# Optimization experiments

Measured on AMD Instinct MI355X. Metric: run time of the kernel, lower is better.

## Reference

```python
import jax, jax.numpy as jnp
import numpy as np

B, L, E, H = 2, 2048, 1024, 16
HD = E // H          # head_dim = 64
G = H // 4           # heads per kernel-size group = 4


def _dwconv(x, w, b):
    """Causal depthwise conv. x: (B, G, L, D); w: (D, k); b: (D,).
    Matches PadLeft(k-1) + Conv1d(D, D, k, groups=D): y[l] = sum_j w[:, j] * x[l - (k-1) + j] + b."""
    k = w.shape[-1]
    Lx = x.shape[2]
    xp = jnp.pad(x, ((0, 0), (0, 0), (k - 1, 0), (0, 0)))
    out = b
    for j in range(k):
        out = out + xp[:, :, j:j + Lx, :] * w[:, j]
    return out


def setup_inputs() -> dict:
    key = jax.random.key(0)
    ks = jax.random.split(key, 32)
    s = 0.02
    inp = {"x": jax.random.normal(ks[0], (B, L, E), jnp.float32)}
    for i, n in enumerate(["Wq", "Wk", "Wv", "Wo"]):
        inp[n] = jax.random.normal(ks[1 + i], (E, E), jnp.float32) * s
    inp["bo"] = jax.random.normal(ks[5], (E,), jnp.float32) * s
    i = 6
    for ksz in (3, 5, 7):
        for pfx in ("q", "k", "v"):
            inp[f"{pfx}{ksz}_w"] = jax.random.normal(ks[i], (HD, ksz), jnp.float32) * (1.0 / ksz)
            inp[f"{pfx}{ksz}_b"] = jax.random.normal(ks[i + 1], (HD,), jnp.float32) * s
            i += 2
    return inp


def reference(x, Wq, Wk, Wv, Wo, bo,
              q3_w, q3_b, k3_w, k3_b, v3_w, v3_b,
              q5_w, q5_b, k5_w, k5_b, v5_w, v5_b,
              q7_w, q7_b, k7_w, k7_b, v7_w, v7_b):
    b, l, _ = x.shape

    def split(t):  # (b, l, E) -> (b, 4, G, l, HD)
        return t.reshape(b, l, 4, G, HD).transpose(0, 2, 3, 1, 4)

    q = split(x @ Wq.T)
    k = split(x @ Wk.T)
    v = split(x @ Wv.T)

    # NOTE: faithful to source quirks -- k and v convs are applied to the
    # (already convolved) q group, not to k/v.
    q0, k0, v0 = q[:, 0], k[:, 0], v[:, 0]
    q1 = _dwconv(q[:, 1], q3_w, q3_b)
    k1 = _dwconv(q1, k3_w, k3_b)
    v1 = _dwconv(q1, v3_w, v3_b)
    q2 = _dwconv(q[:, 2], q5_w, q5_b)
    k2 = _dwconv(q2, k5_w, k5_b)
    v2 = _dwconv(q2, v5_w, v5_b)
    q3 = _dwconv(q[:, 3], q7_w, q7_b)
    k3 = _dwconv(q3, k7_w, k7_b)
    v3 = _dwconv(q3, v7_w, v7_b)

    Q = jnp.concatenate([q0, q1, q2, q3], axis=1)  # (b, H, l, HD)
    K = jnp.concatenate([k0, k1, k2, k3], axis=1)
    V = jnp.concatenate([v0, v1, v2, v3], axis=1)

    logit = jnp.einsum('bnid,bnjd->bnij', Q, K) * (HD ** -0.5)
    attn = jax.nn.softmax(logit, axis=-1)
    attn_out = jnp.einsum('bnij,bnjd->bnid', attn, V)

    # Source quirk: output uses rearranged V, discarding attn_out.
    out = V.transpose(0, 2, 1, 3).reshape(b, l, E)
    # keep the attention compute alive without changing the math
    out = out + 0.0 * attn_out.transpose(0, 2, 1, 3).reshape(b, l, E)
    return out @ Wo.T + bo
```

## Files before the change

kernel.cpp:

```cpp
#include <hip/hip_runtime.h>
#include <hip/hip_bf16.h>
#include <stdint.h>

#define L_SEQ 2048
#define MTOT  4096
#define EDIM  1024

typedef __attribute__((ext_vector_type(8))) short bf16x8;
typedef __attribute__((ext_vector_type(4))) float f32x4;
typedef __attribute__((ext_vector_type(16))) float f32x16;
typedef __attribute__((ext_vector_type(4))) float float4v;
typedef __attribute__((ext_vector_type(4))) unsigned short us4;

__device__ __forceinline__ unsigned short f2b(float f) {
    union { float f; unsigned u; } v; v.f = f;
    return (unsigned short)((v.u + 0x7FFFu + ((v.u >> 16) & 1u)) >> 16);
}
__device__ __forceinline__ float b2f(unsigned short h) {
    union { unsigned u; float f; } v; v.u = ((unsigned)h) << 16;
    return v.f;
}
__device__ __forceinline__ unsigned cvtpk(float lo, float hi) {
    unsigned r;
    asm("v_cvt_pk_bf16_f32 %0, %1, %2" : "=v"(r) : "v"(lo), "v"(hi));
    return r;
}
__device__ __forceinline__ void lds16(const void* g, void* l) {
    __builtin_amdgcn_global_load_lds((const __attribute__((address_space(1))) void*)g,
                                     (__attribute__((address_space(3))) void*)l, 16, 0, 0);
}

__global__ __launch_bounds__(256) void wprep_kernel(
    const float* __restrict__ Wq, const float* __restrict__ Wv,
    const float* __restrict__ Wo,
    unsigned short* __restrict__ W1b, unsigned short* __restrict__ Wob,
    const float* __restrict__ q3w, const float* __restrict__ q3b,
    const float* __restrict__ v3w, const float* __restrict__ v3b,
    const float* __restrict__ q5w, const float* __restrict__ q5b,
    const float* __restrict__ v5w, const float* __restrict__ v5b,
    const float* __restrict__ q7w, const float* __restrict__ q7b,
    const float* __restrict__ v7w, const float* __restrict__ v7b,
    float* __restrict__ H, float* __restrict__ Beff, float* __restrict__ Corr)
{
    if (blockIdx.x >= 2048) {
        int ch = (blockIdx.x - 2048) * 256 + threadIdx.x;
        int g = ch >> 8, d = ch & 63, k = 3 + 2 * g;
        const float* qw = (g == 0) ? q3w : (g == 1) ? q5w : q7w;
        const float* qb = (g == 0) ? q3b : (g == 1) ? q5b : q7b;
        const float* vw = (g == 0) ? v3w : (g == 1) ? v5w : v7w;
        const float* vb = (g == 0) ? v3b : (g == 1) ? v5b : v7b;

        float hq[7], hv[7];
        for (int i = 0; i < 7; ++i) { hq[i] = 0.f; hv[i] = 0.f; }
        for (int i = 0; i < k; ++i) {
            hq[i] = qw[d * k + (k - 1 - i)];
            hv[i] = vw[d * k + (k - 1 - i)];
        }
        float h[13];
        for (int i = 0; i < 13; ++i) h[i] = 0.f;
        for (int a = 0; a < 7; ++a)
            for (int b = 0; b < 7; ++b)
                h[a + b] += hq[a] * hv[b];
        for (int i = 0; i < 13; ++i) H[i * 768 + ch] = h[i];

        float sv = 0.f;
        for (int j = 0; j < k; ++j) sv += vw[d * k + j];
        Beff[ch] = qb[d] * sv + vb[d];

        for (int l = 0; l < 6; ++l) {
            float s2 = 0.f;
            for (int i = l + 1; i < 7; ++i) s2 += hv[i];
            Corr[l * 768 + ch] = qb[d] * s2;
        }
        return;
    }
    const int WQ = (EDIM * EDIM) / 4;
    int i = blockIdx.x * 256 + threadIdx.x;
    const float* src;
    unsigned short* dst;
    int j;
    if (i < WQ) {
        j = i * 4;
        int row = j >> 10;
        src = (row < 256) ? Wv : Wq;
        dst = W1b;
    } else {
        j = (i - WQ) * 4; src = Wo; dst = Wob;
    }
    float4v v = *(const float4v*)(src + j);
    us4 o;
    o[0] = f2b(v[0]); o[1] = f2b(v[1]); o[2] = f2b(v[2]); o[3] = f2b(v[3]);
    *(us4*)(dst + j) = o;
}

__global__ __launch_bounds__(512, 2) void gemm1_fused(
    const float* __restrict__ Af, const unsigned short* __restrict__ BT,
    unsigned short* __restrict__ V,
    const float* __restrict__ H, const float* __restrict__ Beff,
    const float* __restrict__ Corr)
{
    constexpr int ABUF = 49152, ABYT = 32768;
    __shared__ uint8_t sh[3 * ABUF];

    int orig = blockIdx.y * 8 + blockIdx.x;
    int wg   = (orig & 7) * 32 + (orig >> 3);
    const int m0 = (wg >> 3) * 128, n0 = (wg & 7) * 128;
    const bool fir = (n0 >= 256);
    const int  m0h = (m0 == 0) ? 0 : (m0 - 32);
    const int  lbase = m0 & (L_SEQ - 1);

    const int tid  = threadIdx.x;
    const int wid  = tid >> 6;
    const int lane = tid & 63;
    const int wr   = wid >> 2;
    const int wc   = (wid >> 1) & 1;
    const int kh   = wid & 1;
    const int l31  = lane & 31, hi = lane >> 5;
    const bool firw = fir && (wr == 0);

    f32x16 acc[2][2] = {};
    f32x16 hacc[2] = {};

    f32x4 h0s0a = {}, h0s0b = {}, h0s1a = {}, h0s1b = {};
    f32x4 h1s0a = {}, h1s0b = {}, h1s1a = {}, h1s1b = {};
    const float* hrow = Af + (size_t)(m0h + l31) * EDIM + kh * 32 + hi * 8;

#define HALOLOAD(B, t) do { if (firw) {                                     \
        const float* hp = hrow + (t) * 64;                                  \
        h##B##s0a = *(const f32x4*)(hp);      h##B##s0b = *(const f32x4*)(hp + 4);  \
        h##B##s1a = *(const f32x4*)(hp + 16); h##B##s1b = *(const f32x4*)(hp + 20); } } while (0)

    auto stage = [&](int buf, int t) {
        uint8_t* Abase = sh + buf * ABUF;
        uint8_t* Bbase = Abase + ABYT;
        const float* Asrc = Af + (size_t)m0 * EDIM + t * 64;
#pragma unroll
        for (int j = 0; j < 4; ++j) {
            int slot = j * 512 + tid;
            int row = slot >> 4, c = (slot & 15) ^ (row & 15);
            lds16(Asrc + (size_t)row * EDIM + c * 4, Abase + j * 8192 + wid * 1024);
        }
        const unsigned short* Bsrc = BT + (size_t)n0 * EDIM + t * 64;
#pragma unroll
        for (int j = 0; j < 2; ++j) {
            int slot = j * 512 + tid;
            int row = slot >> 3, c = (slot & 7) ^ (row & 7);
            lds16(Bsrc + (size_t)row * EDIM + c * 8, Bbase + j * 8192 + wid * 1024);
        }
    };

    auto compute = [&](int buf, f32x4 hs0a, f32x4 hs0b, f32x4 hs1a, f32x4 hs1b) {
        const uint8_t* Abase = sh + buf * ABUF;
        const unsigned short* bs = (const unsigned short*)(Abase + ABYT);
#pragma unroll
        for (int s = 0; s < 2; ++s) {
            bf16x8 a[2], b[2];
#pragma unroll
            for (int mi = 0; mi < 2; ++mi) {
                int row = wr * 64 + mi * 32 + l31;
                const float* as = (const float*)Abase;
                int c0 = kh * 8 + s * 4 + hi * 2;
                f32x4 lo = *(const f32x4*)(as + row * 64 + ((c0 ^ (row & 15)) * 4));
                f32x4 h4 = *(const f32x4*)(as + row * 64 + (((c0 + 1) ^ (row & 15)) * 4));
                union { unsigned u[4]; bf16x8 v; } fu;
                fu.u[0] = cvtpk(lo[0], lo[1]); fu.u[1] = cvtpk(lo[2], lo[3]);
                fu.u[2] = cvtpk(h4[0], h4[1]); fu.u[3] = cvtpk(h4[2], h4[3]);
                a[mi] = fu.v;
            }
#pragma unroll
            for (int ni = 0; ni < 2; ++ni) {
                int row = wc * 64 + ni * 32 + l31;
                int cg = kh * 4 + s * 2 + hi;
                b[ni] = *(const bf16x8*)(bs + row * 64 + ((cg ^ (row & 7)) * 8));
            }
#pragma unroll
            for (int mi = 0; mi < 2; ++mi)
#pragma unroll
                for (int ni = 0; ni < 2; ++ni)
                    acc[mi][ni] = __builtin_amdgcn_mfma_f32_32x32x16_bf16(a[mi], b[ni], acc[mi][ni], 0, 0, 0);
            if (firw) {
                f32x4 pa = s ? hs1a : hs0a, pb = s ? hs1b : hs0b;
                union { unsigned u[4]; bf16x8 v; } hu;
                hu.u[0] = cvtpk(pa[0], pa[1]); hu.u[1] = cvtpk(pa[2], pa[3]);
                hu.u[2] = cvtpk(pb[0], pb[1]); hu.u[3] = cvtpk(pb[2], pb[3]);
                hacc[0] = __builtin_amdgcn_mfma_f32_32x32x16_bf16(hu.v, b[0], hacc[0], 0, 0, 0);
                hacc[1] = __builtin_amdgcn_mfma_f32_32x32x16_bf16(hu.v, b[1], hacc[1], 0, 0, 0);
            }
        }
    };

    const int NT = EDIM >> 6;
    HALOLOAD(0, 0);
    stage(0, 0);
    stage(1, 1);
    asm volatile("s_waitcnt vmcnt(6)" ::: "memory");
    __builtin_amdgcn_s_barrier();
    asm volatile("" ::: "memory");

    for (int tt = 0; tt < NT; tt += 2) {
        HALOLOAD(1, tt + 1);
        if (tt + 2 < NT) stage((tt + 2) % 3, tt + 2);
        compute(tt % 3, h0s0a, h0s0b, h0s1a, h0s1b);
        if (tt + 2 < NT) asm volatile("s_waitcnt vmcnt(6)" ::: "memory");
        else             asm volatile("s_waitcnt vmcnt(0)" ::: "memory");
        __builtin_amdgcn_s_barrier();
        asm volatile("" ::: "memory");
        if (tt + 2 < NT) HALOLOAD(0, tt + 2);
        if (tt + 3 < NT) stage((tt + 3) % 3, tt + 3);
        compute((tt + 1) % 3, h1s0a, h1s0b, h1s1a, h1s1b);
        if (tt + 2 < NT) {
            if (tt + 3 < NT) asm volatile("s_waitcnt vmcnt(6)" ::: "memory");
            else             asm volatile("s_waitcnt vmcnt(0)" ::: "memory");
            __builtin_amdgcn_s_barrier();
            asm volatile("" ::: "memory");
        }
    }
#undef HALOLOAD

    __syncthreads();
    float* Mg = (float*)sh;
    const int mgbase = (wr * 2 + wc) * 4096;
    if (kh) {
#pragma unroll
        for (int mi = 0; mi < 2; ++mi)
#pragma unroll
            for (int ni = 0; ni < 2; ++ni) {
                int col = ni * 32 + l31;
#pragma unroll
                for (int q = 0; q < 4; ++q) {
                    int grp = mi * 8 + 2 * q + hi;
                    int adr = mgbase + col * 64 + (((grp) ^ (col & 15)) << 2);
                    f32x4 v;
                    v[0] = acc[mi][ni][q * 4 + 0]; v[1] = acc[mi][ni][q * 4 + 1];
                    v[2] = acc[mi][ni][q * 4 + 2]; v[3] = acc[mi][ni][q * 4 + 3];
                    *(f32x4*)(Mg + adr) = v;
                }
            }
        if (firw) {
#pragma unroll
            for (int ni = 0; ni < 2; ++ni) {
                int hcol = ni * 32 + l31;
#pragma unroll
                for (int q = 0; q < 4; ++q) {
                    int hg = 2 * q + hi;
                    int adr = 16384 + wc * 2048 + hcol * 32 + ((hg ^ (hcol & 7)) << 2);
                    f32x4 v;
                    v[0] = hacc[ni][q * 4 + 0]; v[1] = hacc[ni][q * 4 + 1];
                    v[2] = hacc[ni][q * 4 + 2]; v[3] = hacc[ni][q * 4 + 3];
                    *(f32x4*)(Mg + adr) = v;
                }
            }
        }
    }
    __syncthreads();
    if (fir) {
        unsigned short* Tl = (unsigned short*)(sh + 81920);
        if (!kh) {
#pragma unroll
            for (int mi = 0; mi < 2; ++mi)
#pragma unroll
                for (int ni = 0; ni < 2; ++ni) {
                    int col = wc * 64 + ni * 32 + l31;
#pragma unroll
                    for (int q = 0; q < 4; ++q) {
                        int grp = mi * 8 + 2 * q + hi;
                        int adr = mgbase + (ni * 32 + l31) * 64 + (((grp) ^ ((ni * 32 + l31) & 15)) << 2);
                        f32x4 p = *(const f32x4*)(Mg + adr);
                        int Lr = 32 + wr * 64 + mi * 32 + 8 * q + 4 * hi;
                        us4 o;
#pragma unroll
                        for (int j = 0; j < 4; ++j) o[j] = f2b(acc[mi][ni][q * 4 + j] + p[j]);
                        *(us4*)(Tl + col * 172 + Lr) = o;
                    }
                }
            if (wr == 0) {
#pragma unroll
                for (int ni = 0; ni < 2; ++ni) {
                    int hcol = ni * 32 + l31;
                    int col = wc * 64 + hcol;
#pragma unroll
                    for (int q = 0; q < 4; ++q) {
                        int hg = 2 * q + hi;
                        int adr = 16384 + wc * 2048 + hcol * 32 + ((hg ^ (hcol & 7)) << 2);
                        f32x4 p = *(const f32x4*)(Mg + adr);
                        int Lr = 8 * q + 4 * hi;
                        us4 o;
#pragma unroll
                        for (int j = 0; j < 4; ++j) o[j] = f2b(hacc[ni][q * 4 + j] + p[j]);
                        *(us4*)(Tl + col * 172 + Lr) = o;
                    }
                }
            }
        }
        __syncthreads();
        int c = tid & 127, rb = tid >> 7;
        int ch = n0 + c - 256;
        float h[13];
#pragma unroll
        for (int i = 0; i < 13; ++i) h[i] = H[i * 768 + ch];
        float beff = Beff[ch];
        const unsigned short* wp = Tl + c * 172 + 20 + rb * 32;
        float wf[44];
#pragma unroll
        for (int j = 0; j < 11; ++j) {
            us4 t4 = *(const us4*)(wp + j * 4);
            wf[j * 4 + 0] = b2f(t4[0]); wf[j * 4 + 1] = b2f(t4[1]);
            wf[j * 4 + 2] = b2f(t4[2]); wf[j * 4 + 3] = b2f(t4[3]);
        }
        if (lbase == 0 && rb == 0) {
#pragma unroll
            for (int j = 0; j < 12; ++j) wf[j] = 0.f;
        }
        unsigned short* vp = V + (size_t)(m0 + rb * 32) * EDIM + n0 + c;
#pragma unroll
        for (int rr = 0; rr < 32; ++rr) {
            float s = beff;
#pragma unroll
            for (int i = 0; i < 13; ++i) s += h[i] * wf[12 + rr - i];
            int l = lbase + rb * 32 + rr;
            if (l < 6) s -= Corr[l * 768 + ch];
            vp[(size_t)rr * EDIM] = f2b(s);
        }
    } else {
        if (!kh) {
#pragma unroll
            for (int mi = 0; mi < 2; ++mi) {
#pragma unroll
                for (int ni = 0; ni < 2; ++ni) {
                    int col = ni * 32 + l31;
                    int gcol = n0 + wc * 64 + col;
#pragma unroll
                    for (int q = 0; q < 4; ++q) {
                        int grp = mi * 8 + 2 * q + hi;
                        int adr = mgbase + col * 64 + (((grp) ^ (col & 15)) << 2);
                        f32x4 p = *(const f32x4*)(Mg + adr);
                        int rowb = m0 + wr * 64 + mi * 32 + 8 * q + 4 * hi;
#pragma unroll
                        for (int j = 0; j < 4; ++j)
                            V[(size_t)(rowb + j) * EDIM + gcol] = f2b(acc[mi][ni][q * 4 + j] + p[j]);
                    }
                }
            }
        }
    }
}

__global__ __launch_bounds__(512, 2) void gemm2_k(
    const unsigned short* __restrict__ Ab, const unsigned short* __restrict__ BT,
    float* __restrict__ Cf, const float* __restrict__ bias)
{
    constexpr int ABUF = 32768, ABYT = 16384;
    __shared__ uint8_t sh[3 * ABUF];

    int orig = blockIdx.y * 8 + blockIdx.x;
    int wg   = (orig & 7) * 32 + (orig >> 3);
    const int m0 = (wg >> 3) * 128, n0 = (wg & 7) * 128;

    const int tid  = threadIdx.x;
    const int wid  = tid >> 6;
    const int lane = tid & 63;
    const int wr   = wid >> 2;
    const int wc   = (wid >> 1) & 1;
    const int kh   = wid & 1;
    const int l31  = lane & 31, hi = lane >> 5;

    f32x16 acc[2][2] = {};

    auto stage = [&](int buf, int t) {
        uint8_t* Abase = sh + buf * ABUF;
        uint8_t* Bbase = Abase + ABYT;
        const unsigned short* Asrc = Ab + (size_t)m0 * EDIM + t * 64;
#pragma unroll
        for (int j = 0; j < 2; ++j) {
            int slot = j * 512 + tid;
            int row = slot >> 3, c = (slot & 7) ^ (row & 7);
            lds16(Asrc + (size_t)row * EDIM + c * 8, Abase + j * 8192 + wid * 1024);
        }
        const unsigned short* Bsrc = BT + (size_t)n0 * EDIM + t * 64;
#pragma unroll
        for (int j = 0; j < 2; ++j) {
            int slot = j * 512 + tid;
            int row = slot >> 3, c = (slot & 7) ^ (row & 7);
            lds16(Bsrc + (size_t)row * EDIM + c * 8, Bbase + j * 8192 + wid * 1024);
        }
    };

    auto compute = [&](int buf) {
        const uint8_t* Abase = sh + buf * ABUF;
        const unsigned short* as = (const unsigned short*)Abase;
        const unsigned short* bs = (const unsigned short*)(Abase + ABYT);
#pragma unroll
        for (int s = 0; s < 2; ++s) {
            bf16x8 a[2], b[2];
#pragma unroll
            for (int mi = 0; mi < 2; ++mi) {
                int row = wr * 64 + mi * 32 + l31;
                int cg = kh * 4 + s * 2 + hi;
                a[mi] = *(const bf16x8*)(as + row * 64 + ((cg ^ (row & 7)) * 8));
            }
#pragma unroll
            for (int ni = 0; ni < 2; ++ni) {
                int row = wc * 64 + ni * 32 + l31;
                int cg = kh * 4 + s * 2 + hi;
                b[ni] = *(const bf16x8*)(bs + row * 64 + ((cg ^ (row & 7)) * 8));
            }
#pragma unroll
            for (int mi = 0; mi < 2; ++mi)
#pragma unroll
                for (int ni = 0; ni < 2; ++ni)
                    acc[mi][ni] = __builtin_amdgcn_mfma_f32_32x32x16_bf16(a[mi], b[ni], acc[mi][ni], 0, 0, 0);
        }
    };

    const int NT = EDIM >> 6;
    stage(0, 0);
    stage(1, 1);
    asm volatile("s_waitcnt vmcnt(4)" ::: "memory");
    __builtin_amdgcn_s_barrier();
    asm volatile("" ::: "memory");

    for (int t = 0; t < NT; ++t) {
        if (t + 2 < NT) stage((t + 2) % 3, t + 2);
        compute(t % 3);
        if (t + 1 < NT) {
            if (t + 2 < NT) asm volatile("s_waitcnt vmcnt(4)" ::: "memory");
            else            asm volatile("s_waitcnt vmcnt(0)" ::: "memory");
            __builtin_amdgcn_s_barrier();
            asm volatile("" ::: "memory");
        }
    }

    __syncthreads();
    float* Mg = (float*)sh;
    const int mgbase = (wr * 2 + wc) * 4096;
    if (kh) {
#pragma unroll
        for (int mi = 0; mi < 2; ++mi)
#pragma unroll
            for (int ni = 0; ni < 2; ++ni) {
                int col = ni * 32 + l31;
#pragma unroll
                for (int q = 0; q < 4; ++q) {
                    int grp = mi * 8 + 2 * q + hi;
                    int adr = mgbase + col * 64 + (((grp) ^ (col & 15)) << 2);
                    f32x4 v;
                    v[0] = acc[mi][ni][q * 4 + 0]; v[1] = acc[mi][ni][q * 4 + 1];
                    v[2] = acc[mi][ni][q * 4 + 2]; v[3] = acc[mi][ni][q * 4 + 3];
                    *(f32x4*)(Mg + adr) = v;
                }
            }
    }
    __syncthreads();
    if (!kh) {
#pragma unroll
        for (int mi = 0; mi < 2; ++mi) {
#pragma unroll
            for (int ni = 0; ni < 2; ++ni) {
                int col = ni * 32 + l31;
                int gcol = n0 + wc * 64 + col;
#pragma unroll
                for (int q = 0; q < 4; ++q) {
                    int grp = mi * 8 + 2 * q + hi;
                    int adr = mgbase + col * 64 + (((grp) ^ (col & 15)) << 2);
                    f32x4 p = *(const f32x4*)(Mg + adr);
                    int rowb = m0 + wr * 64 + mi * 32 + 8 * q + 4 * hi;
#pragma unroll
                    for (int j = 0; j < 4; ++j)
                        Cf[(size_t)(rowb + j) * EDIM + gcol] = acc[mi][ni][q * 4 + j] + p[j] + bias[gcol];
                }
            }
        }
    }
}

extern "C" void kernel_launch(void* const* d_in, const int* in_sizes, int n_in,
                              void* d_out, int out_size, void* d_ws, size_t ws_size,
                              hipStream_t stream)
{
    const float* x  = (const float*)d_in[0];
    const float* Wq = (const float*)d_in[1];
    const float* Wv = (const float*)d_in[3];
    const float* Wo = (const float*)d_in[4];
    const float* bo = (const float*)d_in[5];

    uint8_t* ws = (uint8_t*)d_ws;
    unsigned short* W1b = (unsigned short*)(ws);
    unsigned short* Wob = (unsigned short*)(ws + (2u  << 20));
    unsigned short* V   = (unsigned short*)(ws + (4u  << 20));
    float* H    = (float*)(ws + (12u << 20));
    float* Beff = (float*)(ws + (12u << 20) + (64u << 10));
    float* Corr = (float*)(ws + (12u << 20) + (96u << 10));

    wprep_kernel<<<2051, 256, 0, stream>>>(
        Wq, Wv, Wo, W1b, Wob,
        (const float*)d_in[6],  (const float*)d_in[7],
        (const float*)d_in[10], (const float*)d_in[11],
        (const float*)d_in[12], (const float*)d_in[13],
        (const float*)d_in[16], (const float*)d_in[17],
        (const float*)d_in[18], (const float*)d_in[19],
        (const float*)d_in[22], (const float*)d_in[23],
        H, Beff, Corr);

    dim3 gg(EDIM / 128, MTOT / 128);
    gemm1_fused<<<gg, 512, 0, stream>>>(x, W1b, V, H, Beff, Corr);

    gemm2_k<<<gg, 512, 0, stream>>>(V, Wob, (float*)d_out, bo);
}
```

Before: 53.85 us.

## Fuse weight bf16 conversion and conv-filter prep into the GEMM kernels

Removes the separate wprep kernel that converted Wq/Wv/Wo to bf16 and precomputed the composed conv filters. gemm1 now loads fp32 weights into registers, converts them to bf16 and writes them to LDS in its software pipeline, and computes the filter taps and bias corrections inline in the epilogue. gemm2 stages fp32 Wo directly into LDS via global_load_lds and converts when reading fragments, which increases its LDS footprint and wait counts. This saves one launch and a pass over the weights, but every tile re-converts weights and moves twice the bytes for the B operand.

```diff
diff --git a/kernel.cpp b/kernel.cpp
--- a/kernel.cpp
+++ b/kernel.cpp
@@ -9,7 +9,6 @@
 typedef __attribute__((ext_vector_type(8))) short bf16x8;
 typedef __attribute__((ext_vector_type(4))) float f32x4;
 typedef __attribute__((ext_vector_type(16))) float f32x16;
-typedef __attribute__((ext_vector_type(4))) float float4v;
 typedef __attribute__((ext_vector_type(4))) unsigned short us4;
 
 __device__ __forceinline__ unsigned short f2b(float f) {
@@ -30,74 +29,16 @@
                                      (__attribute__((address_space(3))) void*)l, 16, 0, 0);
 }
 
-__global__ __launch_bounds__(256) void wprep_kernel(
-    const float* __restrict__ Wq, const float* __restrict__ Wv,
-    const float* __restrict__ Wo,
-    unsigned short* __restrict__ W1b, unsigned short* __restrict__ Wob,
+__global__ __launch_bounds__(512, 2) void gemm1_fused(
+    const float* __restrict__ Af, const float* __restrict__ Wq,
+    const float* __restrict__ Wv,
+    unsigned short* __restrict__ V,
     const float* __restrict__ q3w, const float* __restrict__ q3b,
     const float* __restrict__ v3w, const float* __restrict__ v3b,
     const float* __restrict__ q5w, const float* __restrict__ q5b,
     const float* __restrict__ v5w, const float* __restrict__ v5b,
     const float* __restrict__ q7w, const float* __restrict__ q7b,
-    const float* __restrict__ v7w, const float* __restrict__ v7b,
-    float* __restrict__ H, float* __restrict__ Beff, float* __restrict__ Corr)
-{
-    if (blockIdx.x >= 2048) {
-        int ch = (blockIdx.x - 2048) * 256 + threadIdx.x;
-        int g = ch >> 8, d = ch & 63, k = 3 + 2 * g;
-        const float* qw = (g == 0) ? q3w : (g == 1) ? q5w : q7w;
-        const float* qb = (g == 0) ? q3b : (g == 1) ? q5b : q7b;
-        const float* vw = (g == 0) ? v3w : (g == 1) ? v5w : v7w;
-        const float* vb = (g == 0) ? v3b : (g == 1) ? v5b : v7b;
-
-        float hq[7], hv[7];
-        for (int i = 0; i < 7; ++i) { hq[i] = 0.f; hv[i] = 0.f; }
-        for (int i = 0; i < k; ++i) {
-            hq[i] = qw[d * k + (k - 1 - i)];
-            hv[i] = vw[d * k + (k - 1 - i)];
-        }
-        float h[13];
-        for (int i = 0; i < 13; ++i) h[i] = 0.f;
-        for (int a = 0; a < 7; ++a)
-            for (int b = 0; b < 7; ++b)
-                h[a + b] += hq[a] * hv[b];
-        for (int i = 0; i < 13; ++i) H[i * 768 + ch] = h[i];
-
-        float sv = 0.f;
-        for (int j = 0; j < k; ++j) sv += vw[d * k + j];
-        Beff[ch] = qb[d] * sv + vb[d];
-
-        for (int l = 0; l < 6; ++l) {
-            float s2 = 0.f;
-            for (int i = l + 1; i < 7; ++i) s2 += hv[i];
-            Corr[l * 768 + ch] = qb[d] * s2;
-        }
-        return;
-    }
-    const int WQ = (EDIM * EDIM) / 4;
-    int i = blockIdx.x * 256 + threadIdx.x;
-    const float* src;
-    unsigned short* dst;
-    int j;
-    if (i < WQ) {
-        j = i * 4;
-        int row = j >> 10;
-        src = (row < 256) ? Wv : Wq;
-        dst = W1b;
-    } else {
-        j = (i - WQ) * 4; src = Wo; dst = Wob;
-    }
-    float4v v = *(const float4v*)(src + j);
-    us4 o;
-    o[0] = f2b(v[0]); o[1] = f2b(v[1]); o[2] = f2b(v[2]); o[3] = f2b(v[3]);
-    *(us4*)(dst + j) = o;
-}
-
-__global__ __launch_bounds__(512, 2) void gemm1_fused(
-    const float* __restrict__ Af, const unsigned short* __restrict__ BT,
-    unsigned short* __restrict__ V,
-    const float* __restrict__ H, const float* __restrict__ Beff,
-    const float* __restrict__ Corr)
+    const float* __restrict__ v7w, const float* __restrict__ v7b)
 {
     constexpr int ABUF = 49152, ABYT = 32768;
     __shared__ uint8_t sh[3 * ABUF];
@@ -121,31 +62,53 @@
     f32x16 acc[2][2] = {};
     f32x16 hacc[2] = {};
 
+    const float* Wsrc = (n0 < 256) ? Wv : Wq;
+    const int r0  = tid >> 3, cg0 = tid & 7;
+    const float* Bg0 = Wsrc + (size_t)(n0 + r0) * EDIM + cg0 * 8;
+    const float* Bg1 = Bg0 + (size_t)64 * EDIM;
+    const int dB0 = r0 * 64 + ((cg0 ^ (r0 & 7)) * 8);
+    const int dB1 = (64 + r0) * 64 + ((cg0 ^ (r0 & 7)) * 8);
+    f32x4 bA0_0, bB0_0, bA1_0, bB1_0;
+    f32x4 bA0_1, bB0_1, bA1_1, bB1_1;
+
+#define GLB(BK, t) do {                                                       \
+        bA0_##BK = *(const f32x4*)(Bg0 + (t) * 64);                           \
+        bB0_##BK = *(const f32x4*)(Bg0 + (t) * 64 + 4);                       \
+        bA1_##BK = *(const f32x4*)(Bg1 + (t) * 64);                           \
+        bB1_##BK = *(const f32x4*)(Bg1 + (t) * 64 + 4);                       \
+    } while (0)
+#define DSWB(BK, buf) do {                                                    \
+        unsigned short* Bl = (unsigned short*)(sh + (buf) * ABUF + ABYT);     \
+        union { unsigned u[4]; bf16x8 v; } u0, u1;                            \
+        u0.u[0] = cvtpk(bA0_##BK[0], bA0_##BK[1]);                            \
+        u0.u[1] = cvtpk(bA0_##BK[2], bA0_##BK[3]);                            \
+        u0.u[2] = cvtpk(bB0_##BK[0], bB0_##BK[1]);                            \
+        u0.u[3] = cvtpk(bB0_##BK[2], bB0_##BK[3]);                            \
+        u1.u[0] = cvtpk(bA1_##BK[0], bA1_##BK[1]);                            \
+        u1.u[1] = cvtpk(bA1_##BK[2], bA1_##BK[3]);                            \
+        u1.u[2] = cvtpk(bB1_##BK[0], bB1_##BK[1]);                            \
+        u1.u[3] = cvtpk(bB1_##BK[2], bB1_##BK[3]);                            \
+        *(bf16x8*)(Bl + dB0) = u0.v;                                          \
+        *(bf16x8*)(Bl + dB1) = u1.v;                                          \
+    } while (0)
+
     f32x4 h0s0a = {}, h0s0b = {}, h0s1a = {}, h0s1b = {};
     f32x4 h1s0a = {}, h1s0b = {}, h1s1a = {}, h1s1b = {};
     const float* hrow = Af + (size_t)(m0h + l31) * EDIM + kh * 32 + hi * 8;
 
-#define HALOLOAD(B, t) do { if (firw) {                                     \
-        const float* hp = hrow + (t) * 64;                                  \
+#define HALOLOAD(B, t) do { if (firw) {                                       \
+        const float* hp = hrow + (t) * 64;                                    \
         h##B##s0a = *(const f32x4*)(hp);      h##B##s0b = *(const f32x4*)(hp + 4);  \
         h##B##s1a = *(const f32x4*)(hp + 16); h##B##s1b = *(const f32x4*)(hp + 20); } } while (0)
 
-    auto stage = [&](int buf, int t) {
+    auto stage_a = [&](int buf, int t) {
         uint8_t* Abase = sh + buf * ABUF;
-        uint8_t* Bbase = Abase + ABYT;
         const float* Asrc = Af + (size_t)m0 * EDIM + t * 64;
 #pragma unroll
         for (int j = 0; j < 4; ++j) {
             int slot = j * 512 + tid;
             int row = slot >> 4, c = (slot & 15) ^ (row & 15);
             lds16(Asrc + (size_t)row * EDIM + c * 4, Abase + j * 8192 + wid * 1024);
-        }
-        const unsigned short* Bsrc = BT + (size_t)n0 * EDIM + t * 64;
-#pragma unroll
-        for (int j = 0; j < 2; ++j) {
-            int slot = j * 512 + tid;
-            int row = slot >> 3, c = (slot & 7) ^ (row & 7);
-            lds16(Bsrc + (size_t)row * EDIM + c * 8, Bbase + j * 8192 + wid * 1024);
         }
     };
 
@@ -191,31 +154,43 @@
 
     const int NT = EDIM >> 6;
     HALOLOAD(0, 0);
-    stage(0, 0);
-    stage(1, 1);
-    asm volatile("s_waitcnt vmcnt(6)" ::: "memory");
+    GLB(0, 0);
+    stage_a(0, 0);
+    GLB(1, 1);
+    stage_a(1, 1);
+    DSWB(0, 0);
+    GLB(0, 2);
+    asm volatile("s_waitcnt vmcnt(12) lgkmcnt(0)" ::: "memory");
     __builtin_amdgcn_s_barrier();
     asm volatile("" ::: "memory");
 
     for (int tt = 0; tt < NT; tt += 2) {
         HALOLOAD(1, tt + 1);
-        if (tt + 2 < NT) stage((tt + 2) % 3, tt + 2);
+        if (tt + 2 < NT) stage_a((tt + 2) % 3, tt + 2);
+        if (tt + 1 < NT) DSWB(1, (tt + 1) % 3);
+        if (tt + 3 < NT) GLB(1, tt + 3);
         compute(tt % 3, h0s0a, h0s0b, h0s1a, h0s1b);
-        if (tt + 2 < NT) asm volatile("s_waitcnt vmcnt(6)" ::: "memory");
-        else             asm volatile("s_waitcnt vmcnt(0)" ::: "memory");
-        __builtin_amdgcn_s_barrier();
-        asm volatile("" ::: "memory");
-        if (tt + 2 < NT) HALOLOAD(0, tt + 2);
-        if (tt + 3 < NT) stage((tt + 3) % 3, tt + 3);
+        {
+            if (tt + 3 < NT) asm volatile("s_waitcnt vmcnt(12) lgkmcnt(0)" ::: "memory");
+            else             asm volatile("s_waitcnt vmcnt(0) lgkmcnt(0)" ::: "memory");
+            __builtin_amdgcn_s_barrier();
+            asm volatile("" ::: "memory");
+        }
+        HALOLOAD(0, tt + 2);
+        if (tt + 3 < NT) stage_a((tt + 3) % 3, tt + 3);
+        if (tt + 2 < NT) DSWB(0, (tt + 2) % 3);
+        if (tt + 4 < NT) GLB(0, tt + 4);
         compute((tt + 1) % 3, h1s0a, h1s0b, h1s1a, h1s1b);
         if (tt + 2 < NT) {
-            if (tt + 3 < NT) asm volatile("s_waitcnt vmcnt(6)" ::: "memory");
-            else             asm volatile("s_waitcnt vmcnt(0)" ::: "memory");
+            if (tt + 4 < NT) asm volatile("s_waitcnt vmcnt(12) lgkmcnt(0)" ::: "memory");
+            else             asm volatile("s_waitcnt vmcnt(0) lgkmcnt(0)" ::: "memory");
             __builtin_amdgcn_s_barrier();
             asm volatile("" ::: "memory");
         }
     }
 #undef HALOLOAD
+#undef GLB
+#undef DSWB
 
     __syncthreads();
     float* Mg = (float*)sh;
@@ -295,10 +270,36 @@
         __syncthreads();
         int c = tid & 127, rb = tid >> 7;
         int ch = n0 + c - 256;
+        int g = ch >> 8, d = ch & 63, k = 3 + 2 * g;
+        const float* qw = (g == 0) ? q3w : (g == 1) ? q5w : q7w;
+        const float* qb = (g == 0) ? q3b : (g == 1) ? q5b : q7b;
+        const float* vw = (g == 0) ? v3w : (g == 1) ? v5w : v7w;
+        const float* vb = (g == 0) ? v3b : (g == 1) ? v5b : v7b;
+        float hq[7], hv[7];
+#pragma unroll
+        for (int i = 0; i < 7; ++i) { hq[i] = 0.f; hv[i] = 0.f; }
+        for (int i = 0; i < k; ++i) {
+            hq[i] = qw[d * k + (k - 1 - i)];
+            hv[i] = vw[d * k + (k - 1 - i)];
+        }
         float h[13];
 #pragma unroll
-        for (int i = 0; i < 13; ++i) h[i] = H[i * 768 + ch];
-        float beff = Beff[ch];
+        for (int i = 0; i < 13; ++i) h[i] = 0.f;
+#pragma unroll
+        for (int a = 0; a < 7; ++a)
+#pragma unroll
+            for (int b = 0; b < 7; ++b)
+                h[a + b] += hq[a] * hv[b];
+        float sv = 0.f;
+        for (int j = 0; j < k; ++j) sv += vw[d * k + j];
+        float beff = qb[d] * sv + vb[d];
+        float qbd = qb[d];
+        float csum[6];
+        {
+            float s2 = 0.f;
+#pragma unroll
+            for (int l = 5; l >= 0; --l) { s2 += hv[l + 1]; csum[l] = s2; }
+        }
         const unsigned short* wp = Tl + c * 172 + 20 + rb * 32;
         float wf[44];
 #pragma unroll
@@ -318,7 +319,7 @@
 #pragma unroll
             for (int i = 0; i < 13; ++i) s += h[i] * wf[12 + rr - i];
             int l = lbase + rb * 32 + rr;
-            if (l < 6) s -= Corr[l * 768 + ch];
+            if (l < 6) s -= qbd * csum[l];
             vp[(size_t)rr * EDIM] = f2b(s);
         }
     } else {
@@ -345,11 +346,11 @@
     }
 }
 
-__global__ __launch_bounds__(512, 2) void gemm2_k(
-    const unsigned short* __restrict__ Ab, const unsigned short* __restrict__ BT,
+__global__ __launch_bounds__(512, 2) void gemm2_f(
+    const unsigned short* __restrict__ Ab, const float* __restrict__ Wo,
     float* __restrict__ Cf, const float* __restrict__ bias)
 {
-    constexpr int ABUF = 32768, ABYT = 16384;
+    constexpr int ABUF = 49152, ABYT = 16384;
     __shared__ uint8_t sh[3 * ABUF];
 
     int orig = blockIdx.y * 8 + blockIdx.x;
@@ -376,19 +377,19 @@
             int row = slot >> 3, c = (slot & 7) ^ (row & 7);
             lds16(Asrc + (size_t)row * EDIM + c * 8, Abase + j * 8192 + wid * 1024);
         }
-        const unsigned short* Bsrc = BT + (size_t)n0 * EDIM + t * 64;
-#pragma unroll
-        for (int j = 0; j < 2; ++j) {
+        const float* Bsrc = Wo + (size_t)n0 * EDIM + t * 64;
+#pragma unroll
+        for (int j = 0; j < 4; ++j) {
             int slot = j * 512 + tid;
-            int row = slot >> 3, c = (slot & 7) ^ (row & 7);
-            lds16(Bsrc + (size_t)row * EDIM + c * 8, Bbase + j * 8192 + wid * 1024);
+            int row = slot >> 4, c = (slot & 15) ^ (row & 15);
+            lds16(Bsrc + (size_t)row * EDIM + c * 4, Bbase + j * 8192 + wid * 1024);
         }
     };
 
     auto compute = [&](int buf) {
         const uint8_t* Abase = sh + buf * ABUF;
         const unsigned short* as = (const unsigned short*)Abase;
-        const unsigned short* bs = (const unsigned short*)(Abase + ABYT);
+        const float* bsf = (const float*)(Abase + ABYT);
 #pragma unroll
         for (int s = 0; s < 2; ++s) {
             bf16x8 a[2], b[2];
@@ -401,8 +402,13 @@
 #pragma unroll
             for (int ni = 0; ni < 2; ++ni) {
                 int row = wc * 64 + ni * 32 + l31;
-                int cg = kh * 4 + s * 2 + hi;
-                b[ni] = *(const bf16x8*)(bs + row * 64 + ((cg ^ (row & 7)) * 8));
+                int c0 = kh * 8 + s * 4 + hi * 2;
+                f32x4 lo = *(const f32x4*)(bsf + row * 64 + ((c0 ^ (row & 15)) * 4));
+                f32x4 h4 = *(const f32x4*)(bsf + row * 64 + (((c0 + 1) ^ (row & 15)) * 4));
+                union { unsigned u[4]; bf16x8 v; } fu;
+                fu.u[0] = cvtpk(lo[0], lo[1]); fu.u[1] = cvtpk(lo[2], lo[3]);
+                fu.u[2] = cvtpk(h4[0], h4[1]); fu.u[3] = cvtpk(h4[2], h4[3]);
+                b[ni] = fu.v;
             }
 #pragma unroll
             for (int mi = 0; mi < 2; ++mi)
@@ -415,7 +421,7 @@
     const int NT = EDIM >> 6;
     stage(0, 0);
     stage(1, 1);
-    asm volatile("s_waitcnt vmcnt(4)" ::: "memory");
+    asm volatile("s_waitcnt vmcnt(6)" ::: "memory");
     __builtin_amdgcn_s_barrier();
     asm volatile("" ::: "memory");
 
@@ -423,7 +429,7 @@
         if (t + 2 < NT) stage((t + 2) % 3, t + 2);
         compute(t % 3);
         if (t + 1 < NT) {
-            if (t + 2 < NT) asm volatile("s_waitcnt vmcnt(4)" ::: "memory");
+            if (t + 2 < NT) asm volatile("s_waitcnt vmcnt(6)" ::: "memory");
             else            asm volatile("s_waitcnt vmcnt(0)" ::: "memory");
             __builtin_amdgcn_s_barrier();
             asm volatile("" ::: "memory");
@@ -483,26 +489,17 @@
     const float* Wo = (const float*)d_in[4];
     const float* bo = (const float*)d_in[5];
 
-    uint8_t* ws = (uint8_t*)d_ws;
-    unsigned short* W1b = (unsigned short*)(ws);
-    unsigned short* Wob = (unsigned short*)(ws + (2u  << 20));
-    unsigned short* V   = (unsigned short*)(ws + (4u  << 20));
-    float* H    = (float*)(ws + (12u << 20));
-    float* Beff = (float*)(ws + (12u << 20) + (64u << 10));
-    float* Corr = (float*)(ws + (12u << 20) + (96u << 10));
-
-    wprep_kernel<<<2051, 256, 0, stream>>>(
-        Wq, Wv, Wo, W1b, Wob,
+    unsigned short* V = (unsigned short*)d_ws;
+
+    dim3 gg(EDIM / 128, MTOT / 128);
+    gemm1_fused<<<gg, 512, 0, stream>>>(
+        x, Wq, Wv, V,
         (const float*)d_in[6],  (const float*)d_in[7],
         (const float*)d_in[10], (const float*)d_in[11],
         (const float*)d_in[12], (const float*)d_in[13],
         (const float*)d_in[16], (const float*)d_in[17],
         (const float*)d_in[18], (const float*)d_in[19],
-        (const float*)d_in[22], (const float*)d_in[23],
-        H, Beff, Corr);
-
-    dim3 gg(EDIM / 128, MTOT / 128);
-    gemm1_fused<<<gg, 512, 0, stream>>>(x, W1b, V, H, Beff, Corr);
-
-    gemm2_k<<<gg, 512, 0, stream>>>(V, Wob, (float*)d_out, bo);
-}
+        (const float*)d_in[22], (const float*)d_in[23]);
+
+    gemm2_f<<<gg, 512, 0, stream>>>(V, Wo, (float*)d_out, bo);
+}
```

After: 55.10 us. 2.3% more time.
